# Performance work log

Measured on AMD Instinct MI355X. Metric: run time of the kernel, lower is better.

The kernel has to match this reference:

```python
import jax, jax.numpy as jnp
import numpy as np

B, L, H = 32, 256, 384
MAX_WAVE = 2048  # config.max_wave_length


def setup_inputs() -> dict:
    key = jax.random.key(0)
    k1, k2 = jax.random.split(key)
    encoder_hidden_states = jax.random.normal(k1, (B, L, H), dtype=jnp.float32)
    durations_gt = jax.random.randint(k2, (B, L), 0, 15, dtype=jnp.int32)
    return {"encoder_hidden_states": encoder_hidden_states, "durations_gt": durations_gt}


def reference(encoder_hidden_states, durations_gt):
    # Length regulation: token i is repeated durations_gt[b, i] times along the
    # output frame axis; frames past the total length are zero-padded.
    csum = jnp.cumsum(durations_gt, axis=1)               # [B, L] inclusive cumsum
    total = csum[:, -1]                                    # [B] real lengths
    t = jnp.arange(MAX_WAVE, dtype=csum.dtype)             # [T]
    # frame t belongs to token idx where csum[idx-1] <= t < csum[idx]
    idx = jax.vmap(lambda c: jnp.searchsorted(c, t, side="right"))(csum)  # [B, T]
    valid = t[None, :] < total[:, None]                    # [B, T]
    safe_idx = jnp.clip(idx, 0, L - 1)
    gathered = jnp.take_along_axis(encoder_hidden_states, safe_idx[..., None], axis=1)  # [B, T, H]
    gathered = jnp.where(valid[..., None], gathered, 0.0)
    outputs = jnp.transpose(gathered, (0, 2, 1))           # [B, H, T] per custom-op output shape
    encoder_masks = valid.astype(encoder_hidden_states.dtype)  # [B, T]
    return outputs, encoder_masks
```

## Files before the change

kernel.cpp:

```cpp
#include <hip/hip_runtime.h>

constexpr int Lc = 256;
constexpr int Hc = 384;
constexpr int Tc = 2048;
constexpr int Bc = 32;
constexpr int T_PER_BLOCK = 1024;
constexpr int H_TILE = 16;
constexpr int PADW = 17;

__global__ __launch_bounds__(256) void lr_expand_kernel(
    const float* __restrict__ enc,
    const int*   __restrict__ dur,
    float*       __restrict__ out,
    float*       __restrict__ mask)
{
    const int tid = threadIdx.x;
    const int b   = blockIdx.z;
    const int h0  = blockIdx.y * H_TILE;

    __shared__ int   s_csum[Lc];
    __shared__ float s_enc[Lc * PADW];

    {
        const float* encb = enc + (size_t)b * (Lc * Hc) + h0;
        const int r  = tid >> 2;
        const int c4 = (tid & 3) * 4;
#pragma unroll
        for (int it = 0; it < 4; ++it) {
            const int row = r + it * 64;
            float4 v = *reinterpret_cast<const float4*>(encb + (size_t)row * Hc + c4);
            float* dst = s_enc + row * PADW + c4;
            dst[0] = v.x; dst[1] = v.y; dst[2] = v.z; dst[3] = v.w;
        }
    }

    s_csum[tid] = dur[b * Lc + tid];
    __syncthreads();
#pragma unroll
    for (int off = 1; off < Lc; off <<= 1) {
        int v = (tid >= off) ? s_csum[tid - off] : 0;
        __syncthreads();
        s_csum[tid] += v;
        __syncthreads();
    }
    const int total = s_csum[Lc - 1];

    const int tbase = blockIdx.x * T_PER_BLOCK + tid * 4;

    int   rowoff[4];
    float mflag[4];
    {
        int lo = 0, hi = Lc;
        while (lo < hi) {
            int mid = (lo + hi) >> 1;
            if (s_csum[mid] <= tbase) lo = mid + 1; else hi = mid;
        }
        int cur = lo;
#pragma unroll
        for (int k = 0; k < 4; ++k) {
            const int tt = tbase + k;
            while (cur < Lc && s_csum[cur] <= tt) cur++;
            const int safe = (cur < Lc - 1) ? cur : (Lc - 1);
            rowoff[k] = safe * PADW;
            mflag[k]  = (tt < total) ? 1.0f : 0.0f;
        }
    }

    float* outb = out + (size_t)b * (Hc * Tc) + (size_t)h0 * Tc + tbase;
#pragma unroll
    for (int hh = 0; hh < H_TILE; ++hh) {
        float4 v;
        v.x = s_enc[rowoff[0] + hh] * mflag[0];
        v.y = s_enc[rowoff[1] + hh] * mflag[1];
        v.z = s_enc[rowoff[2] + hh] * mflag[2];
        v.w = s_enc[rowoff[3] + hh] * mflag[3];
        *reinterpret_cast<float4*>(outb + (size_t)hh * Tc) = v;
    }

    if (blockIdx.y == 0) {
        float4 m;
        m.x = mflag[0]; m.y = mflag[1]; m.z = mflag[2]; m.w = mflag[3];
        *reinterpret_cast<float4*>(mask + (size_t)b * Tc + tbase) = m;
    }
}

extern "C" void kernel_launch(void* const* d_in, const int* in_sizes, int n_in,
                              void* d_out, int out_size, void* d_ws, size_t ws_size,
                              hipStream_t stream) {
    const float* enc = (const float*)d_in[0];
    const int*   dur = (const int*)d_in[1];

    float* out  = (float*)d_out;
    float* mask = out + (size_t)Bc * Hc * Tc;

    dim3 grid(Tc / T_PER_BLOCK, Hc / H_TILE, Bc);
    dim3 block(256);
    lr_expand_kernel<<<grid, block, 0, stream>>>(enc, dur, out, mask);
}
```

Measured before the change: 27.28 us.

## Precompute per-batch frame indices in a separate kernel before expansion

Moves the prefix sum and searchsorted into a small per-batch kernel that writes packed 16-bit row indices with a validity bit, plus the mask, to workspace. The expansion kernel then reads those indices instead of redoing the scan and binary search in every H-tile block, which removes 24x redundant scan work and its barriers. The cost is an extra launch and a dependency between the two kernels. A fused fallback remains for the case where the workspace is too small.

Result: slower. 32.23 us (+18.1%).

```diff
diff --git a/kernel.cpp b/kernel.cpp
--- a/kernel.cpp
+++ b/kernel.cpp
@@ -8,17 +8,70 @@
 constexpr int H_TILE = 16;
 constexpr int PADW = 17;
 
+__global__ __launch_bounds__(256) void lr_index_kernel(
+    const int*      __restrict__ dur,
+    unsigned short* __restrict__ idx16,
+    float*          __restrict__ mask)
+{
+    const int tid = threadIdx.x;
+    const int b   = blockIdx.x;
+
+    __shared__ int s_csum[Lc];
+    s_csum[tid] = dur[b * Lc + tid];
+    __syncthreads();
+#pragma unroll
+    for (int off = 1; off < Lc; off <<= 1) {
+        int v = (tid >= off) ? s_csum[tid - off] : 0;
+        __syncthreads();
+        s_csum[tid] += v;
+        __syncthreads();
+    }
+    const int total = s_csum[Lc - 1];
+
+    const int t0 = tid * 8;
+    int lo = 0, hi = Lc;
+    while (lo < hi) {
+        int mid = (lo + hi) >> 1;
+        if (s_csum[mid] <= t0) lo = mid + 1; else hi = mid;
+    }
+    int cur = lo;
+
+    unsigned int packed[4];
+    float mv[8];
+#pragma unroll
+    for (int p = 0; p < 4; ++p) {
+        unsigned int w = 0;
+#pragma unroll
+        for (int q = 0; q < 2; ++q) {
+            const int k  = p * 2 + q;
+            const int tt = t0 + k;
+            while (cur < Lc && s_csum[cur] <= tt) cur++;
+            const int safe  = (cur < Lc - 1) ? cur : (Lc - 1);
+            const bool valid = (tt < total);
+            unsigned int enc = (unsigned int)safe | (valid ? 0u : 0x8000u);
+            w |= enc << (16 * q);
+            mv[k] = valid ? 1.0f : 0.0f;
+        }
+        packed[p] = w;
+    }
+
+    uint4 iv; iv.x = packed[0]; iv.y = packed[1]; iv.z = packed[2]; iv.w = packed[3];
+    *reinterpret_cast<uint4*>(idx16 + (size_t)b * Tc + t0) = iv;
+    float4 m0; m0.x = mv[0]; m0.y = mv[1]; m0.z = mv[2]; m0.w = mv[3];
+    float4 m1; m1.x = mv[4]; m1.y = mv[5]; m1.z = mv[6]; m1.w = mv[7];
+    *reinterpret_cast<float4*>(mask + (size_t)b * Tc + t0)     = m0;
+    *reinterpret_cast<float4*>(mask + (size_t)b * Tc + t0 + 4) = m1;
+}
+
 __global__ __launch_bounds__(256) void lr_expand_kernel(
-    const float* __restrict__ enc,
-    const int*   __restrict__ dur,
-    float*       __restrict__ out,
-    float*       __restrict__ mask)
+    const float*          __restrict__ enc,
+    const unsigned short* __restrict__ idx16,
+    float*                __restrict__ out)
 {
     const int tid = threadIdx.x;
     const int b   = blockIdx.z;
     const int h0  = blockIdx.y * H_TILE;
 
-    __shared__ int   s_csum[Lc];
     __shared__ float s_enc[Lc * PADW];
 
     {
@@ -34,6 +87,54 @@
         }
     }
 
+    const int tbase = blockIdx.x * T_PER_BLOCK + tid * 4;
+    ushort4 iv = *reinterpret_cast<const ushort4*>(idx16 + (size_t)b * Tc + tbase);
+
+    int   rowoff[4];
+    float mflag[4];
+    rowoff[0] = (int)(iv.x & 0xff) * PADW; mflag[0] = (iv.x & 0x8000) ? 0.0f : 1.0f;
+    rowoff[1] = (int)(iv.y & 0xff) * PADW; mflag[1] = (iv.y & 0x8000) ? 0.0f : 1.0f;
+    rowoff[2] = (int)(iv.z & 0xff) * PADW; mflag[2] = (iv.z & 0x8000) ? 0.0f : 1.0f;
+    rowoff[3] = (int)(iv.w & 0xff) * PADW; mflag[3] = (iv.w & 0x8000) ? 0.0f : 1.0f;
+
+    __syncthreads();
+
+    float* outb = out + (size_t)b * (Hc * Tc) + (size_t)h0 * Tc + tbase;
+#pragma unroll
+    for (int hh = 0; hh < H_TILE; ++hh) {
+        float4 v;
+        v.x = s_enc[rowoff[0] + hh] * mflag[0];
+        v.y = s_enc[rowoff[1] + hh] * mflag[1];
+        v.z = s_enc[rowoff[2] + hh] * mflag[2];
+        v.w = s_enc[rowoff[3] + hh] * mflag[3];
+        *reinterpret_cast<float4*>(outb + (size_t)hh * Tc) = v;
+    }
+}
+
+__global__ __launch_bounds__(256) void lr_fused_kernel(
+    const float* __restrict__ enc, const int* __restrict__ dur,
+    float* __restrict__ out, float* __restrict__ mask)
+{
+    const int tid = threadIdx.x;
+    const int b   = blockIdx.z;
+    const int h0  = blockIdx.y * H_TILE;
+
+    __shared__ int   s_csum[Lc];
+    __shared__ float s_enc[Lc * PADW];
+
+    {
+        const float* encb = enc + (size_t)b * (Lc * Hc) + h0;
+        const int r  = tid >> 2;
+        const int c4 = (tid & 3) * 4;
+#pragma unroll
+        for (int it = 0; it < 4; ++it) {
+            const int row = r + it * 64;
+            float4 v = *reinterpret_cast<const float4*>(encb + (size_t)row * Hc + c4);
+            float* dst = s_enc + row * PADW + c4;
+            dst[0] = v.x; dst[1] = v.y; dst[2] = v.z; dst[3] = v.w;
+        }
+    }
+
     s_csum[tid] = dur[b * Lc + tid];
     __syncthreads();
 #pragma unroll
@@ -46,7 +147,6 @@
     const int total = s_csum[Lc - 1];
 
     const int tbase = blockIdx.x * T_PER_BLOCK + tid * 4;
-
     int   rowoff[4];
     float mflag[4];
     {
@@ -93,7 +193,15 @@
     float* out  = (float*)d_out;
     float* mask = out + (size_t)Bc * Hc * Tc;
 
-    dim3 grid(Tc / T_PER_BLOCK, Hc / H_TILE, Bc);
-    dim3 block(256);
-    lr_expand_kernel<<<grid, block, 0, stream>>>(enc, dur, out, mask);
-}
+    const size_t idx_bytes = (size_t)Bc * Tc * sizeof(unsigned short);
+
+    if (ws_size >= idx_bytes) {
+        unsigned short* idx16 = (unsigned short*)d_ws;
+        lr_index_kernel<<<Bc, 256, 0, stream>>>(dur, idx16, mask);
+        dim3 grid(Tc / T_PER_BLOCK, Hc / H_TILE, Bc);
+        lr_expand_kernel<<<grid, dim3(256), 0, stream>>>(enc, idx16, out);
+    } else {
+        dim3 grid(Tc / T_PER_BLOCK, Hc / H_TILE, Bc);
+        lr_fused_kernel<<<grid, dim3(256), 0, stream>>>(enc, dur, out, mask);
+    }
+}
```

## Replace LDS scan and binary search with wave-shuffle scan and scatter-built row map

Applied to the files above, without the earlier changes.

Computes the duration prefix sum with wave shuffles plus a four-entry cross-wave combine, replacing the barrier-heavy LDS Hillis-Steele scan. Each token then writes its own index over its frame range into a shared ushort map, which removes the per-thread binary search and linear walk. Global loads of the encoder tile are issued into registers before the scan so they overlap it, and output stores become nontemporal. The scatter loop's length depends on the duration (up to 14 here), and unfilled frames default to index 255.

Result: no change. 26.96 us (-1.2%).

```diff
diff --git a/kernel.cpp b/kernel.cpp
--- a/kernel.cpp
+++ b/kernel.cpp
@@ -8,79 +8,94 @@
 constexpr int H_TILE = 16;
 constexpr int PADW = 17;
 
-__global__ __launch_bounds__(256) void lr_expand_kernel(
+typedef float  floatx4 __attribute__((ext_vector_type(4)));
+
+__global__ __launch_bounds__(256) void lr_fused_kernel(
     const float* __restrict__ enc,
     const int*   __restrict__ dur,
     float*       __restrict__ out,
     float*       __restrict__ mask)
 {
-    const int tid = threadIdx.x;
-    const int b   = blockIdx.z;
-    const int h0  = blockIdx.y * H_TILE;
+    const int tid  = threadIdx.x;
+    const int lane = tid & 63;
+    const int wv   = tid >> 6;
+    const int b    = blockIdx.z;
+    const int h0   = blockIdx.y * H_TILE;
 
-    __shared__ int   s_csum[Lc];
-    __shared__ float s_enc[Lc * PADW];
+    __shared__ float          s_enc[Lc * PADW];
+    __shared__ unsigned short s_row[Tc];
+    __shared__ int            s_wtot[4];
 
+    const float* encb = enc + (size_t)b * (Lc * Hc) + h0;
+    const int r  = tid >> 2;
+    const int c4 = (tid & 3) * 4;
+    floatx4 st[4];
+#pragma unroll
+    for (int it = 0; it < 4; ++it)
+        st[it] = *reinterpret_cast<const floatx4*>(encb + (size_t)(r + it * 64) * Hc + c4);
+
+    const int d = dur[b * Lc + tid];
     {
-        const float* encb = enc + (size_t)b * (Lc * Hc) + h0;
-        const int r  = tid >> 2;
-        const int c4 = (tid & 3) * 4;
-#pragma unroll
-        for (int it = 0; it < 4; ++it) {
-            const int row = r + it * 64;
-            float4 v = *reinterpret_cast<const float4*>(encb + (size_t)row * Hc + c4);
-            float* dst = s_enc + row * PADW + c4;
-            dst[0] = v.x; dst[1] = v.y; dst[2] = v.z; dst[3] = v.w;
-        }
+        uint4 f;
+        f.x = 0x00FF00FFu; f.y = 0x00FF00FFu; f.z = 0x00FF00FFu; f.w = 0x00FF00FFu;
+        *reinterpret_cast<uint4*>(s_row + tid * 8) = f;
     }
 
-    s_csum[tid] = dur[b * Lc + tid];
+    int s = d;
+#pragma unroll
+    for (int off = 1; off < 64; off <<= 1) {
+        int t = __shfl_up(s, off);
+        if (lane >= off) s += t;
+    }
+    if (lane == 63) s_wtot[wv] = s;
+
+#pragma unroll
+    for (int it = 0; it < 4; ++it) {
+        float* dst = s_enc + (r + it * 64) * PADW + c4;
+        dst[0] = st[it].x; dst[1] = st[it].y; dst[2] = st[it].z; dst[3] = st[it].w;
+    }
+
     __syncthreads();
+
+    int pre = 0, total = 0;
 #pragma unroll
-    for (int off = 1; off < Lc; off <<= 1) {
-        int v = (tid >= off) ? s_csum[tid - off] : 0;
-        __syncthreads();
-        s_csum[tid] += v;
-        __syncthreads();
+    for (int w = 0; w < 4; ++w) {
+        int t = s_wtot[w];
+        total += t;
+        if (w < wv) pre += t;
     }
-    const int total = s_csum[Lc - 1];
+    const int csum_i = s + pre;
+    const int excl   = csum_i - d;
+    int hiw = csum_i; if (hiw > Tc) hiw = Tc;
+    for (int t = excl; t < hiw; ++t) s_row[t] = (unsigned short)tid;
+
+    __syncthreads();
 
     const int tbase = blockIdx.x * T_PER_BLOCK + tid * 4;
+    ushort4 iv = *reinterpret_cast<const ushort4*>(s_row + tbase);
 
     int   rowoff[4];
     float mflag[4];
-    {
-        int lo = 0, hi = Lc;
-        while (lo < hi) {
-            int mid = (lo + hi) >> 1;
-            if (s_csum[mid] <= tbase) lo = mid + 1; else hi = mid;
-        }
-        int cur = lo;
-#pragma unroll
-        for (int k = 0; k < 4; ++k) {
-            const int tt = tbase + k;
-            while (cur < Lc && s_csum[cur] <= tt) cur++;
-            const int safe = (cur < Lc - 1) ? cur : (Lc - 1);
-            rowoff[k] = safe * PADW;
-            mflag[k]  = (tt < total) ? 1.0f : 0.0f;
-        }
-    }
+    rowoff[0] = (int)iv.x * PADW; mflag[0] = (tbase + 0 < total) ? 1.0f : 0.0f;
+    rowoff[1] = (int)iv.y * PADW; mflag[1] = (tbase + 1 < total) ? 1.0f : 0.0f;
+    rowoff[2] = (int)iv.z * PADW; mflag[2] = (tbase + 2 < total) ? 1.0f : 0.0f;
+    rowoff[3] = (int)iv.w * PADW; mflag[3] = (tbase + 3 < total) ? 1.0f : 0.0f;
 
     float* outb = out + (size_t)b * (Hc * Tc) + (size_t)h0 * Tc + tbase;
 #pragma unroll
     for (int hh = 0; hh < H_TILE; ++hh) {
-        float4 v;
+        floatx4 v;
         v.x = s_enc[rowoff[0] + hh] * mflag[0];
         v.y = s_enc[rowoff[1] + hh] * mflag[1];
         v.z = s_enc[rowoff[2] + hh] * mflag[2];
         v.w = s_enc[rowoff[3] + hh] * mflag[3];
-        *reinterpret_cast<float4*>(outb + (size_t)hh * Tc) = v;
+        __builtin_nontemporal_store(v, reinterpret_cast<floatx4*>(outb + (size_t)hh * Tc));
     }
 
     if (blockIdx.y == 0) {
-        float4 m;
+        floatx4 m;
         m.x = mflag[0]; m.y = mflag[1]; m.z = mflag[2]; m.w = mflag[3];
-        *reinterpret_cast<float4*>(mask + (size_t)b * Tc + tbase) = m;
+        __builtin_nontemporal_store(m, reinterpret_cast<floatx4*>(mask + (size_t)b * Tc + tbase));
     }
 }
 
@@ -95,5 +110,5 @@
 
     dim3 grid(Tc / T_PER_BLOCK, Hc / H_TILE, Bc);
     dim3 block(256);
-    lr_expand_kernel<<<grid, block, 0, stream>>>(enc, dur, out, mask);
+    lr_fused_kernel<<<grid, block, 0, stream>>>(enc, dur, out, mask);
 }
```
